# Optimization experiments

Hardware: AMD Instinct MI355X
Metric: run time of the kernel (lower is better)

## Reference

```python
import jax, jax.numpy as jnp
import numpy as np

# dims
B, F, K = 64, 4096, 8
D_IN = D_SLOT = D_KVQ = 192
HID = 768
N_ITERS = 3
EPS = 1e-8
GROUPS = [(0, 1), (1, 7), (7, 8)]  # bg / fg / ag contiguous slot slices
SB_STRENGTH = 1.0
SB_SIGMA = 0.25
GRID = 64  # sqrt(F)


def _layernorm(x, g, b):
    m = jnp.mean(x, axis=-1, keepdims=True)
    v = jnp.mean(jnp.square(x - m), axis=-1, keepdims=True)
    return (x - m) * jax.lax.rsqrt(v + 1e-5) * g + b


def _gru_cell(x, h, Wih, Whh, bih, bhh):
    # torch.nn.GRUCell semantics; gate order r, z, n
    gi = x @ Wih.T + bih
    gh = h @ Whh.T + bhh
    ir, iz, i_n = jnp.split(gi, 3, axis=-1)
    hr, hz, h_n = jnp.split(gh, 3, axis=-1)
    r = jax.nn.sigmoid(ir + hr)
    z = jax.nn.sigmoid(iz + hz)
    n = jnp.tanh(i_n + r * h_n)
    return (1.0 - z) * n + z * h


def _token_coords():
    y = np.linspace(-1.0, 1.0, GRID, dtype=np.float32)
    x = np.linspace(-1.0, 1.0, GRID, dtype=np.float32)
    yy, xx = np.meshgrid(y, x, indexing='ij')
    return jnp.asarray(np.stack((xx, yy), axis=-1).reshape(F, 2))


def setup_inputs() -> dict:
    key = jax.random.key(0)
    ks = jax.random.split(key, 16)
    def n(i, shape, s=0.02):
        return jax.random.normal(ks[i], shape, jnp.float32) * s
    return dict(
        features=jax.random.normal(ks[0], (B, F, D_IN), jnp.float32),
        slots=jax.random.normal(ks[1], (B, K, D_SLOT), jnp.float32),
        Wk=n(2, (D_IN, D_KVQ)), Wv=n(3, (D_IN, D_KVQ)), Wq=n(4, (D_SLOT, D_KVQ)),
        ln_feat_g=jnp.ones(D_IN), ln_feat_b=jnp.zeros(D_IN),
        ln_slot_g=jnp.ones(D_SLOT), ln_slot_b=jnp.zeros(D_SLOT),
        gru_Wih=n(5, (3, 3 * D_SLOT, D_KVQ)), gru_Whh=n(6, (3, 3 * D_SLOT, D_SLOT)),
        gru_bih=n(7, (3, 3 * D_SLOT)), gru_bhh=n(8, (3, 3 * D_SLOT)),
        mlp_ln_g=jnp.ones((3, D_SLOT)), mlp_ln_b=jnp.zeros((3, D_SLOT)),
        mlp_W1=n(9, (3, D_SLOT, HID)), mlp_b1=n(10, (3, HID)),
        mlp_W2=n(11, (3, HID, D_SLOT)), mlp_b2=n(12, (3, D_SLOT)),
    )


def reference(features, slots, Wk, Wv, Wq, ln_feat_g, ln_feat_b, ln_slot_g,
              ln_slot_b, gru_Wih, gru_Whh, gru_bih, gru_bhh, mlp_ln_g,
              mlp_ln_b, mlp_W1, mlp_b1, mlp_W2, mlp_b2):
    coords = _token_coords()  # (F, 2)
    f = _layernorm(features, ln_feat_g, ln_feat_b)
    k = f @ Wk  # (B, F, Dk)
    v = f @ Wv
    scale = D_KVQ ** -0.5
    sigma2 = max(SB_SIGMA ** 2, 1e-8)
    prev_attn = None
    for _ in range(N_ITERS):
        slots_prev = slots
        q = _layernorm(slots, ln_slot_g, ln_slot_b) @ Wq  # (B, K, Dk)
        dots = jnp.einsum('bkd,bfd->bkf', q, k) * scale
        if prev_attn is not None and SB_STRENGTH > 0.0:
            w = prev_attn / (prev_attn.sum(-1, keepdims=True) + 1e-8)
            centers = jnp.einsum('bkf,fd->bkd', w, coords)  # (B, K, 2)
            diff = coords[None, None] - centers[:, :, None]  # (B, K, F, 2)
            dist2 = jnp.sum(diff * diff, axis=-1)
            dots = dots + SB_STRENGTH * (-dist2 / (2.0 * sigma2))
        attn = jax.nn.softmax(dots, axis=1)  # competition over slots
        prev_attn = attn
        w = attn / (attn.sum(-1, keepdims=True) + EPS)  # weighted mean over F
        updates = jnp.einsum('bkf,bfd->bkd', w, v)  # (B, K, Dk)
        outs = []
        for g, (s, e) in enumerate(GROUPS):
            u = updates[:, s:e].reshape(-1, D_KVQ)
            h_prev = slots_prev[:, s:e].reshape(-1, D_SLOT)
            h = _gru_cell(u, h_prev, gru_Wih[g], gru_Whh[g], gru_bih[g], gru_bhh[g])
            x = _layernorm(h, mlp_ln_g[g], mlp_ln_b[g])
            x = jax.nn.relu(x @ mlp_W1[g] + mlp_b1[g]) @ mlp_W2[g] + mlp_b2[g]
            outs.append((h + x).reshape(B, e - s, D_SLOT))
        slots = jnp.concatenate(outs, axis=1)
    return slots
```

## Files before the change

### kernel.cpp

```cpp
#include <hip/hip_runtime.h>

typedef unsigned short u16;
typedef unsigned int u32;

#define BB 64
#define FF 4096
#define DD 192
#define HH 768

typedef __attribute__((ext_vector_type(8))) __bf16 bf16x8;
typedef __attribute__((ext_vector_type(4))) float f32x4;

__device__ __forceinline__ float bf2f(u32 u) {
  union { u32 i; float f; } x; x.i = u << 16; return x.f;
}
__device__ __forceinline__ u16 f2bf(float f) {
  __bf16 h = (__bf16)f;
  return __builtin_bit_cast(u16, h);
}
__device__ __forceinline__ u32 pk2bf(float a, float b) {
  return (u32)f2bf(a) | ((u32)f2bf(b) << 16);
}
__device__ __forceinline__ float sigm(float x) { return 1.f / (1.f + __expf(-x)); }

__global__ void prep_vw(const float* __restrict__ Wk, const float* __restrict__ Wv,
                        const float* __restrict__ g, const float* __restrict__ bb,
                        float* __restrict__ Wvm, float* __restrict__ s0v,
                        float* __restrict__ s0k) {
  int d = threadIdx.x;
  float av = 0.f, ak = 0.f;
  for (int e = 0; e < DD; ++e) {
    float wv = Wv[e * DD + d];
    Wvm[e * DD + d] = g[e] * wv;
    av += bb[e] * wv;
    ak += bb[e] * Wk[e * DD + d];
  }
  s0v[d] = av; s0k[d] = ak;
}

__global__ void prep_packw(const float* __restrict__ Wih, const float* __restrict__ Whh,
                           const float* __restrict__ W1, const float* __restrict__ W2,
                           u16* __restrict__ pWih, u16* __restrict__ pWhh,
                           u16* __restrict__ pW1, u16* __restrict__ pW2) {
  int which = blockIdx.y;
  int total, N, E;
  const float* src; u16* dst; int srcEmajor;
  if (which < 2) { total = 3 * 576 * 192; N = 576; E = 192; srcEmajor = 0;
                   src = which ? Whh : Wih; dst = which ? pWhh : pWih; }
  else if (which == 2) { total = 3 * 192 * 768; N = 768; E = 192; srcEmajor = 1;
                         src = W1; dst = pW1; }
  else { total = 3 * 768 * 192; N = 192; E = 768; srcEmajor = 1; src = W2; dst = pW2; }
  for (int idx = blockIdx.x * 256 + threadIdx.x; idx < total; idx += gridDim.x * 256) {
    int g = idx / (N * E), rem = idx % (N * E);
    int n, e;
    if (srcEmajor) { e = rem / N; n = rem % N; }
    else { n = rem / E; e = rem % E; }
    dst[((g * (E / 2) + (e >> 1)) * N + n) * 2 + (e & 1)] = f2bf(src[idx]);
  }
}

__global__ __launch_bounds__(256) void fconv(const float* __restrict__ feat,
                                             u16* __restrict__ fb, u16* __restrict__ fd,
                                             float2* __restrict__ stats) {
  __shared__ __align__(16) u16 flds[64 * 192];
  int tid = threadIdx.x;
  int blk = blockIdx.x;
  int r = tid >> 2, p = tid & 3;
  long t = (long)blk * 64 + r;
  const float4* src = (const float4*)(feat + t * DD) + p * 12;
  float s = 0.f, s2 = 0.f;
  long Tg = t >> 4; int tau = (int)(t & 15);
  #pragma unroll
  for (int i = 0; i < 6; ++i) {
    float4 a = src[i * 2], b = src[i * 2 + 1];
    s += a.x + a.y + a.z + a.w + b.x + b.y + b.z + b.w;
    s2 += a.x * a.x + a.y * a.y + a.z * a.z + a.w * a.w +
          b.x * b.x + b.y * b.y + b.z * b.z + b.w * b.w;
    uint4 v;
    v.x = pk2bf(a.x, a.y); v.y = pk2bf(a.z, a.w);
    v.z = pk2bf(b.x, b.y); v.w = pk2bf(b.z, b.w);
    int u = p * 6 + i;
    *(uint4*)(fb + ((Tg * 24 + u) * 16 + tau) * 8) = v;
    *(uint4*)((char*)flds + r * 384 + p * 96 + i * 16) = v;
  }
  s += __shfl_xor(s, 1); s2 += __shfl_xor(s2, 1);
  s += __shfl_xor(s, 2); s2 += __shfl_xor(s2, 2);
  if (p == 0) {
    float mu = s * (1.f / 192.f);
    float rstd = rsqrtf(s2 * (1.f / 192.f) - mu * mu + 1e-5f);
    stats[t] = make_float2(rstd, mu);
  }
  __syncthreads();
  int b = blk >> 6;
  #pragma unroll
  for (int i = 0; i < 6; ++i) {
    int idx = tid + i * 256;
    int tg8 = idx / 192, d = idx % 192;
    u16 h[8];
    #pragma unroll
    for (int j = 0; j < 8; ++j) h[j] = flds[(tg8 * 8 + j) * 192 + d];
    uint4 v;
    v.x = (u32)h[0] | ((u32)h[1] << 16);
    v.y = (u32)h[2] | ((u32)h[3] << 16);
    v.z = (u32)h[4] | ((u32)h[5] << 16);
    v.w = (u32)h[6] | ((u32)h[7] << 16);
    int g32 = (blk & 63) * 2 + (tg8 >> 2);
    int l4f = tg8 & 3;
    *(uint4*)(fd + ((((long)b * 128 + g32) * 12 + (d >> 4)) * 64 + l4f * 16 +
                    (d & 15)) * 8) = v;
  }
}

__global__ __launch_bounds__(64) void qproj_kernel(
    const float* __restrict__ slots, const float* __restrict__ Wq,
    const float* __restrict__ lsg, const float* __restrict__ lsb,
    const float* __restrict__ Wk, const float* __restrict__ lfg,
    const float* __restrict__ s0k,
    u16* __restrict__ pbuf, float* __restrict__ pab,
    float* __restrict__ U, float* __restrict__ scal_cur) {
  __shared__ float ln[192];
  int bk = blockIdx.x;
  int b = bk >> 3, sl = bk & 7;
  int lane = threadIdx.x;
  {
    int gtid = bk * 64 + lane;
    float4 z = {0.f, 0.f, 0.f, 0.f};
    if (gtid < 24576) ((float4*)U)[gtid] = z;
    else if (gtid < 24576 + 512) ((float4*)scal_cur)[gtid - 24576] = z;
  }
  const float* x = slots + bk * DD;
  float v0 = x[lane], v1 = x[lane + 64], v2 = x[lane + 128];
  float s = v0 + v1 + v2, s2 = v0 * v0 + v1 * v1 + v2 * v2;
  #pragma unroll
  for (int m = 1; m < 64; m <<= 1) { s += __shfl_xor(s, m); s2 += __shfl_xor(s2, m); }
  float mu = s * (1.f / 192.f);
  float rstd = rsqrtf(s2 * (1.f / 192.f) - mu * mu + 1e-5f);
  ln[lane]       = (v0 - mu) * rstd * lsg[lane]       + lsb[lane];
  ln[lane + 64]  = (v1 - mu) * rstd * lsg[lane + 64]  + lsb[lane + 64];
  ln[lane + 128] = (v2 - mu) * rstd * lsg[lane + 128] + lsb[lane + 128];
  __syncthreads();
  float a0 = 0.f, a1 = 0.f, a2 = 0.f;
  for (int e = 0; e < DD; ++e) {
    float le = ln[e];
    a0 += le * Wq[e * DD + lane];
    a1 += le * Wq[e * DD + lane + 64];
    a2 += le * Wq[e * DD + lane + 128];
  }
  __syncthreads();
  const float scale = 0.07216878364870323f;
  ln[lane] = a0 * scale; ln[lane + 64] = a1 * scale; ln[lane + 128] = a2 * scale;
  __syncthreads();
  float al = 0.f, be = 0.f;
  u16 pb[3];
  #pragma unroll
  for (int k3 = 0; k3 < 3; ++k3) {
    int d = lane + k3 * 64;
    const float* wr = Wk + (size_t)d * DD;
    float pd = 0.f;
    for (int e = 0; e < DD; ++e) pd += wr[e] * ln[e];
    pd *= lfg[d];
    u16 h = f2bf(pd);
    pb[k3] = h;
    al += bf2f(h);
    be += s0k[d] * ln[d];
  }
  #pragma unroll
  for (int m = 1; m < 64; m <<= 1) { al += __shfl_xor(al, m); be += __shfl_xor(be, m); }
  #pragma unroll
  for (int k3 = 0; k3 < 3; ++k3)
    pbuf[(b * 16 + sl) * DD + lane + k3 * 64] = pb[k3];
  if (lane < 24) *(uint4*)(pbuf + (b * 16 + 8 + sl) * DD + lane * 8) = (uint4){0, 0, 0, 0};
  if (lane == 0) { pab[bk * 2] = al; pab[bk * 2 + 1] = be; }
}

__global__ __launch_bounds__(256) void attnpv_kernel(
    const u16* __restrict__ fb, const u16* __restrict__ fd,
    const u16* __restrict__ pbuf, const float* __restrict__ pab,
    const float2* __restrict__ stats,
    const float* __restrict__ scal_prev,
    float* __restrict__ U, float* __restrict__ scal_cur, int have_bias) {
  __shared__ __align__(16) u16 plds[16 * 192];
  __shared__ __align__(16) u16 attn_lds[16 * 256];
  int b = blockIdx.x;
  int chunk = blockIdx.y * 256;
  int tid = threadIdx.x;
  #pragma unroll
  for (int i = 0; i < 2; ++i) {
    int g = tid + i * 256;
    if (g < 384) {
      int s = g / 24, u = g % 24;
      uint4 v = *(const uint4*)(pbuf + ((b * 16 + s) * DD + u * 8));
      *(uint4*)((char*)plds + s * 384 + ((u ^ (s & 7)) << 4)) = v;
    }
  }
  *(uint4*)((char*)attn_lds + 4096 + tid * 16) = (uint4){0, 0, 0, 0};
  __syncthreads();
  int w = tid >> 6, lane = tid & 63;
  int l15 = lane & 15, l4 = lane >> 4;
  bf16x8 qfr[6];
  #pragma unroll
  for (int kk = 0; kk < 6; ++kk) {
    int u = kk * 4 + l4;
    qfr[kk] = *(bf16x8*)((char*)plds + l15 * 384 + ((u ^ (l15 & 7)) << 4));
  }
  float ax[4], ay[4], c0[4], av[4], bv[4];
  #pragma unroll
  for (int j = 0; j < 4; ++j) {
    int s = l4 * 4 + j;
    if (s < 8) {
      av[j] = pab[(b * 8 + s) * 2];
      bv[j] = pab[(b * 8 + s) * 2 + 1];
      if (have_bias) {
        float inv = 1.f / (scal_prev[(b * 8 + s) * 4] + 1e-8f);
        float cx = scal_prev[(b * 8 + s) * 4 + 1] * inv;
        float cy = scal_prev[(b * 8 + s) * 4 + 2] * inv;
        ax[j] = 16.f * cx; ay[j] = 16.f * cy; c0[j] = -8.f * (cx * cx + cy * cy);
      } else { ax[j] = 0.f; ay[j] = 0.f; c0[j] = 0.f; }
    } else { av[j] = 0.f; bv[j] = 0.f; ax[j] = 0.f; ay[j] = 0.f; c0[j] = 0.f; }
  }
  float pa[4], px[4], py[4], pg[4];
  #pragma unroll
  for (int j = 0; j < 4; ++j) { pa[j] = 0.f; px[j] = 0.f; py[j] = 0.f; pg[j] = 0.f; }
  for (int tile = w; tile < 16; tile += 4) {
    int t0 = chunk + tile * 16;
    long Tg = (long)b * 256 + (t0 >> 4);
    const u16* kp = fb + (Tg * 24 + l4) * 128 + l15 * 8;
    f32x4 acc = (f32x4){0.f, 0.f, 0.f, 0.f};
    #pragma unroll
    for (int kk = 0; kk < 6; ++kk) {
      bf16x8 bfr = *(const bf16x8*)(kp + kk * 512);
      acc = __builtin_amdgcn_mfma_f32_16x16x32_bf16(qfr[kk], bfr, acc, 0, 0, 0);
    }
    int t = t0 + l15;
    float2 st = stats[((long)b << 12) + t];
    float rstd = st.x, muv = st.y;
    float x = -1.f + (float)(t & 63) * (2.f / 63.f);
    float y = -1.f + (float)(t >> 6) * (2.f / 63.f);
    float m8r2 = -8.f * (x * x + y * y);
    float d4[4];
    #pragma unroll
    for (int j = 0; j < 4; ++j)
      d4[j] = rstd * acc[j] - rstd * muv * av[j] + bv[j] +
              (have_bias ? (ax[j] * x + ay[j] * y + c0[j] + m8r2) : 0.f);
    float o4[4];
    #pragma unroll
    for (int j = 0; j < 4; ++j) o4[j] = __shfl_xor(d4[j], 16);
    float mx = fmaxf(fmaxf(fmaxf(d4[0], d4[1]), fmaxf(d4[2], d4[3])),
                     fmaxf(fmaxf(o4[0], o4[1]), fmaxf(o4[2], o4[3])));
    float e4[4];
    float sum = 0.f;
    #pragma unroll
    for (int j = 0; j < 4; ++j) { e4[j] = __expf(d4[j] - mx); sum += e4[j]; }
    #pragma unroll
    for (int j = 0; j < 4; ++j) sum += __expf(o4[j] - mx);
    float inv = 1.f / sum;
    if (l4 < 2) {
      int tl = tile * 16 + l15;
      #pragma unroll
      for (int j = 0; j < 4; ++j) {
        float a = e4[j] * inv;
        u16 wr = f2bf(a * rstd);
        int s = l4 * 4 + j;
        *(u16*)((char*)attn_lds + ((s * 512 + tl * 2) ^ ((s & 7) << 4))) = wr;
        pa[j] += a; px[j] += a * x; py[j] += a * y;
        pg[j] += bf2f(wr) * muv;
      }
    }
  }
  #pragma unroll
  for (int m = 1; m < 16; m <<= 1) {
    #pragma unroll
    for (int j = 0; j < 4; ++j) {
      pa[j] += __shfl_xor(pa[j], m);
      px[j] += __shfl_xor(px[j], m);
      py[j] += __shfl_xor(py[j], m);
      pg[j] += __shfl_xor(pg[j], m);
    }
  }
  if (l15 == 0 && l4 < 2) {
    #pragma unroll
    for (int j = 0; j < 4; ++j) {
      int s = l4 * 4 + j;
      atomicAdd(&scal_cur[(b * 8 + s) * 4], pa[j]);
      atomicAdd(&scal_cur[(b * 8 + s) * 4 + 1], px[j]);
      atomicAdd(&scal_cur[(b * 8 + s) * 4 + 2], py[j]);
      atomicAdd(&scal_cur[(b * 8 + s) * 4 + 3], pg[j]);
    }
  }
  __syncthreads();
  int g32base = chunk >> 5;
  #pragma unroll
  for (int ni = 0; ni < 3; ++ni) {
    int nt = w * 3 + ni;
    f32x4 acc = (f32x4){0.f, 0.f, 0.f, 0.f};
    const u16* vp = fd + ((((long)b * 128 + g32base) * 12 + nt) * 64 + l4 * 16 + l15) * 8;
    #pragma unroll
    for (int gl = 0; gl < 8; ++gl) {
      int tl0 = gl * 32 + l4 * 8;
      bf16x8 afr = *(bf16x8*)((char*)attn_lds + ((l15 * 512 + tl0 * 2) ^ ((l15 & 7) << 4)));
      bf16x8 bfr = *(const bf16x8*)(vp + gl * 12 * 64 * 8);
      acc = __builtin_amdgcn_mfma_f32_16x16x32_bf16(afr, bfr, acc, 0, 0, 0);
    }
    if (l4 < 2) {
      #pragma unroll
      for (int j = 0; j < 4; ++j) {
        int s = l4 * 4 + j;
        atomicAdd(&U[((long)b * 8 + s) * DD + nt * 16 + l15], acc[j]);
      }
    }
  }
}

template <int M>
__device__ void gru_body(int b0, int g, int srow,
                         float* u_l, float* h_l, float* gi_l, float* gh_l,
                         float* hn_l, float* ln_l, float* x1_l, float* out_l, float* st,
                         const float* __restrict__ U, const float* __restrict__ scal,
                         const float* __restrict__ Wvm, const float* __restrict__ s0v,
                         const float* __restrict__ sin_,
                         const u16* __restrict__ pWih, const u16* __restrict__ pWhh,
                         const float* __restrict__ bih, const float* __restrict__ bhh,
                         const float* __restrict__ mlng, const float* __restrict__ mlnb,
                         const u16* __restrict__ pW1, const float* __restrict__ b1,
                         const u16* __restrict__ pW2, const float* __restrict__ b2,
                         float* __restrict__ sout) {
  int tid = threadIdx.x;
  for (int idx = tid; idx < M * 192; idx += 768) {
    int row = idx / 192, d = idx % 192;
    int gr = b0 * 8 + srow + row;
    hn_l[row * 192 + d] = U[(long)gr * DD + d];
    h_l[row * 192 + d] = sin_[gr * DD + d];
  }
  __syncthreads();
  if (tid < M * 192) {
    int row = tid / 192, d = tid % 192;
    int gr = b0 * 8 + srow + row;
    float asum = scal[gr * 4], gam = scal[gr * 4 + 3];
    float inv = 1.f / (asum + 1e-8f);
    float acc = asum * s0v[d];
    const float* ur = hn_l + row * 192;
    #pragma unroll 4
    for (int e = 0; e < DD; ++e) acc += (ur[e] - gam) * Wvm[e * DD + d];
    u_l[row * 192 + d] = acc * inv;
  }
  __syncthreads();
  if (tid < 576) {
    int c = tid;
    const u16* wih = pWih + (size_t)g * 96 * 1152 + c * 2;
    const u16* whh = pWhh + (size_t)g * 96 * 1152 + c * 2;
    float ai[M], ah[M];
    #pragma unroll
    for (int r = 0; r < M; ++r) { ai[r] = 0.f; ah[r] = 0.f; }
    #pragma unroll 4
    for (int e2 = 0; e2 < 96; ++e2) {
      u32 wi = *(const u32*)(wih + e2 * 1152);
      u32 wh = *(const u32*)(whh + e2 * 1152);
      float wi0 = bf2f(wi & 0xffffu), wi1 = bf2f(wi >> 16);
      float wh0 = bf2f(wh & 0xffffu), wh1 = bf2f(wh >> 16);
      #pragma unroll
      for (int r = 0; r < M; ++r) {
        ai[r] += wi0 * u_l[r * 192 + e2 * 2] + wi1 * u_l[r * 192 + e2 * 2 + 1];
        ah[r] += wh0 * h_l[r * 192 + e2 * 2] + wh1 * h_l[r * 192 + e2 * 2 + 1];
      }
    }
    #pragma unroll
    for (int r = 0; r < M; ++r) { gi_l[r * 576 + c] = ai[r]; gh_l[r * 576 + c] = ah[r]; }
  }
  __syncthreads();
  if (tid < M * 192) {
    int row = tid / 192, uu = tid % 192;
    const float* bihg = bih + g * 576;
    const float* bhhg = bhh + g * 576;
    float r_ = sigm(gi_l[row * 576 + uu] + bihg[uu] + gh_l[row * 576 + uu] + bhhg[uu]);
    float z_ = sigm(gi_l[row * 576 + 192 + uu] + bihg[192 + uu] +
                    gh_l[row * 576 + 192 + uu] + bhhg[192 + uu]);
    float nn = gi_l[row * 576 + 384 + uu] + bihg[384 + uu] +
               r_ * (gh_l[row * 576 + 384 + uu] + bhhg[384 + uu]);
    float t = 1.f - 2.f / (__expf(2.f * nn) + 1.f);
    hn_l[row * 192 + uu] = (1.f - z_) * t + z_ * h_l[row * 192 + uu];
  }
  __syncthreads();
  {
    int wv = tid >> 6, lane = tid & 63;
    if (wv < M) {
      float v0 = hn_l[wv * 192 + lane], v1 = hn_l[wv * 192 + lane + 64],
            v2 = hn_l[wv * 192 + lane + 128];
      float s = v0 + v1 + v2, sq = v0 * v0 + v1 * v1 + v2 * v2;
      #pragma unroll
      for (int m = 1; m < 64; m <<= 1) { s += __shfl_xor(s, m); sq += __shfl_xor(sq, m); }
      if (lane == 0) {
        float mu = s * (1.f / 192.f);
        st[wv * 2] = mu;
        st[wv * 2 + 1] = rsqrtf(sq * (1.f / 192.f) - mu * mu + 1e-5f);
      }
    }
  }
  __syncthreads();
  if (tid < M * 192) {
    int row = tid / 192, uu = tid % 192;
    ln_l[row * 192 + uu] = (hn_l[row * 192 + uu] - st[row * 2]) * st[row * 2 + 1] *
                               mlng[g * DD + uu] + mlnb[g * DD + uu];
  }
  __syncthreads();
  {
    int c = tid;
    const u16* w1 = pW1 + (size_t)g * 96 * 1536 + c * 2;
    float a[M];
    #pragma unroll
    for (int r = 0; r < M; ++r) a[r] = 0.f;
    #pragma unroll 4
    for (int e2 = 0; e2 < 96; ++e2) {
      u32 wp = *(const u32*)(w1 + e2 * 1536);
      float w0 = bf2f(wp & 0xffffu), w1f = bf2f(wp >> 16);
      #pragma unroll
      for (int r = 0; r < M; ++r)
        a[r] += w0 * ln_l[r * 192 + e2 * 2] + w1f * ln_l[r * 192 + e2 * 2 + 1];
    }
    float bc = b1[g * HH + c];
    #pragma unroll
    for (int r = 0; r < M; ++r) x1_l[r * 768 + c] = fmaxf(a[r] + bc, 0.f);
  }
  if (tid < M * 192) {
    int row = tid / 192, uu = tid % 192;
    out_l[row * 192 + uu] = hn_l[row * 192 + uu] + b2[g * DD + uu];
  }
  __syncthreads();
  {
    int c = tid % 192, ks = tid / 192;
    const u16* w2 = pW2 + (size_t)g * 384 * 384 + c * 2;
    float a[M];
    #pragma unroll
    for (int r = 0; r < M; ++r) a[r] = 0.f;
    #pragma unroll 4
    for (int e2 = ks * 96; e2 < ks * 96 + 96; ++e2) {
      u32 wp = *(const u32*)(w2 + e2 * 384);
      float w0 = bf2f(wp & 0xffffu), w1f = bf2f(wp >> 16);
      #pragma unroll
      for (int r = 0; r < M; ++r)
        a[r] += w0 * x1_l[r * 768 + e2 * 2] + w1f * x1_l[r * 768 + e2 * 2 + 1];
    }
    #pragma unroll
    for (int r = 0; r < M; ++r) atomicAdd(&out_l[r * 192 + c], a[r]);
  }
  __syncthreads();
  if (tid < M * 192) {
    int row = tid / 192, d = tid % 192;
    sout[(b0 * 8 + srow + row) * DD + d] = out_l[row * 192 + d];
  }
}

__global__ __launch_bounds__(768) void gru_kernel(
    const float* __restrict__ U, const float* __restrict__ scal,
    const float* __restrict__ Wvm, const float* __restrict__ s0v,
    const float* __restrict__ sin_,
    const u16* __restrict__ pWih, const u16* __restrict__ pWhh,
    const float* __restrict__ bih, const float* __restrict__ bhh,
    const float* __restrict__ mlng, const float* __restrict__ mlnb,
    const u16* __restrict__ pW1, const float* __restrict__ b1,
    const u16* __restrict__ pW2, const float* __restrict__ b2,
    float* __restrict__ sout) {
  __shared__ float u_l[3 * 192], h_l[3 * 192], gi_l[3 * 576], gh_l[3 * 576];
  __shared__ float hn_l[3 * 192], ln_l[3 * 192], x1_l[3 * 768], out_l[3 * 192], st[8];
  int b = blockIdx.x, y = blockIdx.y;
  if (y == 0)
    gru_body<1>(b, 0, 0, u_l, h_l, gi_l, gh_l, hn_l, ln_l, x1_l, out_l, st,
                U, scal, Wvm, s0v, sin_, pWih, pWhh, bih, bhh, mlng, mlnb,
                pW1, b1, pW2, b2, sout);
  else if (y == 1)
    gru_body<1>(b, 2, 7, u_l, h_l, gi_l, gh_l, hn_l, ln_l, x1_l, out_l, st,
                U, scal, Wvm, s0v, sin_, pWih, pWhh, bih, bhh, mlng, mlnb,
                pW1, b1, pW2, b2, sout);
  else if (y == 2)
    gru_body<3>(b, 1, 1, u_l, h_l, gi_l, gh_l, hn_l, ln_l, x1_l, out_l, st,
                U, scal, Wvm, s0v, sin_, pWih, pWhh, bih, bhh, mlng, mlnb,
                pW1, b1, pW2, b2, sout);
  else
    gru_body<3>(b, 1, 4, u_l, h_l, gi_l, gh_l, hn_l, ln_l, x1_l, out_l, st,
                U, scal, Wvm, s0v, sin_, pWih, pWhh, bih, bhh, mlng, mlnb,
                pW1, b1, pW2, b2, sout);
}

extern "C" void kernel_launch(void* const* d_in, const int* in_sizes, int n_in,
                              void* d_out, int out_size, void* d_ws, size_t ws_size,
                              hipStream_t stream) {
  const float* feat = (const float*)d_in[0];
  const float* slots = (const float*)d_in[1];
  const float* Wk = (const float*)d_in[2];
  const float* Wv = (const float*)d_in[3];
  const float* Wq = (const float*)d_in[4];
  const float* lfg = (const float*)d_in[5];
  const float* lfb = (const float*)d_in[6];
  const float* lsg = (const float*)d_in[7];
  const float* lsb = (const float*)d_in[8];
  const float* gWih = (const float*)d_in[9];
  const float* gWhh = (const float*)d_in[10];
  const float* gbih = (const float*)d_in[11];
  const float* gbhh = (const float*)d_in[12];
  const float* mlng = (const float*)d_in[13];
  const float* mlnb = (const float*)d_in[14];
  const float* W1 = (const float*)d_in[15];
  const float* b1 = (const float*)d_in[16];
  const float* W2 = (const float*)d_in[17];
  const float* b2 = (const float*)d_in[18];
  float* out = (float*)d_out;

  char* ws = (char*)d_ws;
  size_t off = 0;
  auto alloc = [&](size_t bytes) {
    void* p = ws + off;
    off += (bytes + 255) & ~(size_t)255;
    return p;
  };
  u16* fb      = (u16*)alloc((size_t)BB * FF * DD * 2);
  u16* fd      = (u16*)alloc((size_t)BB * DD * FF * 2);
  float2* stats = (float2*)alloc((size_t)BB * FF * 8);
  u16* pbuf    = (u16*)alloc((size_t)BB * 16 * DD * 2);
  float* pab   = (float*)alloc((size_t)BB * 8 * 2 * 4);
  float* U     = (float*)alloc((size_t)BB * 8 * DD * 4);
  float* slA   = (float*)alloc((size_t)BB * 8 * DD * 4);
  float* slB   = (float*)alloc((size_t)BB * 8 * DD * 4);
  float* scal0 = (float*)alloc(BB * 8 * 4 * 4);
  float* scal1 = (float*)alloc(BB * 8 * 4 * 4);
  float* Wvm   = (float*)alloc((size_t)DD * DD * 4);
  float* s0v   = (float*)alloc(DD * 4);
  float* s0k   = (float*)alloc(DD * 4);
  u16* pWih    = (u16*)alloc((size_t)3 * 576 * DD * 2);
  u16* pWhh    = (u16*)alloc((size_t)3 * 576 * DD * 2);
  u16* pW1     = (u16*)alloc((size_t)3 * DD * HH * 2);
  u16* pW2     = (u16*)alloc((size_t)3 * HH * DD * 2);

  prep_vw<<<1, 192, 0, stream>>>(Wk, Wv, lfg, lfb, Wvm, s0v, s0k);
  prep_packw<<<dim3(432, 4), 256, 0, stream>>>(gWih, gWhh, W1, W2, pWih, pWhh, pW1, pW2);
  fconv<<<BB * FF / 64, 256, 0, stream>>>(feat, fb, fd, stats);

  const float* sin_ = slots;
  float* souts[3] = {slA, slB, out};
  float* scals[2] = {scal0, scal1};
  for (int it = 0; it < 3; ++it) {
    int cur = it & 1, prev = cur ^ 1;
    qproj_kernel<<<BB * 8, 64, 0, stream>>>(sin_, Wq, lsg, lsb, Wk, lfg, s0k,
                                            pbuf, pab, U, scals[cur]);
    attnpv_kernel<<<dim3(BB, 16), 256, 0, stream>>>(fb, fd, pbuf, pab, stats,
                                                    scals[prev], U, scals[cur],
                                                    it > 0 ? 1 : 0);
    gru_kernel<<<dim3(BB, 4), 768, 0, stream>>>(U, scals[cur], Wvm, s0v, sin_,
                                                pWih, pWhh, gbih, gbhh, mlng, mlnb,
                                                pW1, b1, pW2, b2, souts[it]);
    sin_ = souts[it];
  }
}
```

Measured before the change: 519.2 us.

## Fuse first-iteration attention and PV into feature conversion kernel

Merges the first slot-attention iteration (logits, softmax over slots, attention-weighted value accumulation, centroid scalars) into the feature bf16 conversion kernel, so the freshly converted 64-token tile in LDS is reused instead of re-read from global memory. The first qproj launch is moved before the conversion kernel, and the remaining iterations always apply the spatial bias, so the have_bias flag is dropped. In exchange, the fused kernel uses more LDS and registers and adds more atomics per block into U and the scalar buffers.

Result: slower. 774.7 us (+49.2%).

```diff
diff --git a/kernel.cpp b/kernel.cpp
--- a/kernel.cpp
+++ b/kernel.cpp
@@ -59,55 +59,180 @@
   }
 }
 
-__global__ __launch_bounds__(256) void fconv(const float* __restrict__ feat,
-                                             u16* __restrict__ fb, u16* __restrict__ fd,
-                                             float2* __restrict__ stats) {
+__global__ __launch_bounds__(256) void fconv_attn1(
+    const float* __restrict__ feat, u16* __restrict__ fb, u16* __restrict__ fd,
+    float2* __restrict__ stats, const u16* __restrict__ pbuf,
+    const float* __restrict__ pab, float* __restrict__ U,
+    float* __restrict__ scal_cur) {
   __shared__ __align__(16) u16 flds[64 * 192];
+  __shared__ __align__(16) u16 plds[16 * 192];
+  __shared__ __align__(16) u16 attn_lds[16 * 64];
+  __shared__ float stat_l[64 * 2];
   int tid = threadIdx.x;
   int blk = blockIdx.x;
-  int r = tid >> 2, p = tid & 3;
-  long t = (long)blk * 64 + r;
-  const float4* src = (const float4*)(feat + t * DD) + p * 12;
-  float s = 0.f, s2 = 0.f;
-  long Tg = t >> 4; int tau = (int)(t & 15);
+  int b = blk >> 6;
+  int w = tid >> 6, lane = tid & 63;
+  int l15 = lane & 15, l4 = lane >> 4;
+  #pragma unroll
+  for (int i = 0; i < 2; ++i) {
+    int g = tid + i * 256;
+    if (g < 384) {
+      int s = g / 24, u = g % 24;
+      uint4 v = *(const uint4*)(pbuf + ((b * 16 + s) * DD + u * 8));
+      *(uint4*)((char*)plds + s * 384 + ((u ^ (s & 7)) << 4)) = v;
+    }
+  }
+  if (tid < 64) *(uint4*)((char*)attn_lds + 1024 + tid * 16) = (uint4){0, 0, 0, 0};
+  {
+    int r = tid >> 2, p = tid & 3;
+    long t = (long)blk * 64 + r;
+    const float4* src = (const float4*)(feat + t * DD) + p * 12;
+    float s = 0.f, s2 = 0.f;
+    long Tg = t >> 4; int tau = (int)(t & 15);
+    #pragma unroll
+    for (int i = 0; i < 6; ++i) {
+      float4 a = src[i * 2], c = src[i * 2 + 1];
+      s += a.x + a.y + a.z + a.w + c.x + c.y + c.z + c.w;
+      s2 += a.x * a.x + a.y * a.y + a.z * a.z + a.w * a.w +
+            c.x * c.x + c.y * c.y + c.z * c.z + c.w * c.w;
+      uint4 v;
+      v.x = pk2bf(a.x, a.y); v.y = pk2bf(a.z, a.w);
+      v.z = pk2bf(c.x, c.y); v.w = pk2bf(c.z, c.w);
+      int u = p * 6 + i;
+      *(uint4*)(fb + ((Tg * 24 + u) * 16 + tau) * 8) = v;
+      *(uint4*)((char*)flds + r * 384 + ((u ^ (r & 7)) << 4)) = v;
+    }
+    s += __shfl_xor(s, 1); s2 += __shfl_xor(s2, 1);
+    s += __shfl_xor(s, 2); s2 += __shfl_xor(s2, 2);
+    if (p == 0) {
+      float mu = s * (1.f / 192.f);
+      float rstd = rsqrtf(s2 * (1.f / 192.f) - mu * mu + 1e-5f);
+      stats[t] = make_float2(rstd, mu);
+      stat_l[r * 2] = rstd; stat_l[r * 2 + 1] = mu;
+    }
+  }
+  __syncthreads();
+  uint4 gran[6];
   #pragma unroll
   for (int i = 0; i < 6; ++i) {
-    float4 a = src[i * 2], b = src[i * 2 + 1];
-    s += a.x + a.y + a.z + a.w + b.x + b.y + b.z + b.w;
-    s2 += a.x * a.x + a.y * a.y + a.z * a.z + a.w * a.w +
-          b.x * b.x + b.y * b.y + b.z * b.z + b.w * b.w;
-    uint4 v;
-    v.x = pk2bf(a.x, a.y); v.y = pk2bf(a.z, a.w);
-    v.z = pk2bf(b.x, b.y); v.w = pk2bf(b.z, b.w);
-    int u = p * 6 + i;
-    *(uint4*)(fb + ((Tg * 24 + u) * 16 + tau) * 8) = v;
-    *(uint4*)((char*)flds + r * 384 + p * 96 + i * 16) = v;
-  }
-  s += __shfl_xor(s, 1); s2 += __shfl_xor(s2, 1);
-  s += __shfl_xor(s, 2); s2 += __shfl_xor(s2, 2);
-  if (p == 0) {
-    float mu = s * (1.f / 192.f);
-    float rstd = rsqrtf(s2 * (1.f / 192.f) - mu * mu + 1e-5f);
-    stats[t] = make_float2(rstd, mu);
-  }
-  __syncthreads();
-  int b = blk >> 6;
-  #pragma unroll
-  for (int i = 0; i < 6; ++i) {
-    int idx = tid + i * 256;
-    int tg8 = idx / 192, d = idx % 192;
+    int pair = w * 6 + i;
+    int nt = pair >> 1, ks = pair & 1;
+    int d = nt * 16 + l15;
     u16 h[8];
     #pragma unroll
-    for (int j = 0; j < 8; ++j) h[j] = flds[(tg8 * 8 + j) * 192 + d];
+    for (int j = 0; j < 8; ++j) {
+      int tok = ks * 32 + l4 * 8 + j;
+      h[j] = *(const u16*)((char*)flds + tok * 384 +
+                           (((d >> 3) ^ (tok & 7)) << 4) + (d & 7) * 2);
+    }
     uint4 v;
     v.x = (u32)h[0] | ((u32)h[1] << 16);
     v.y = (u32)h[2] | ((u32)h[3] << 16);
     v.z = (u32)h[4] | ((u32)h[5] << 16);
     v.w = (u32)h[6] | ((u32)h[7] << 16);
-    int g32 = (blk & 63) * 2 + (tg8 >> 2);
-    int l4f = tg8 & 3;
-    *(uint4*)(fd + ((((long)b * 128 + g32) * 12 + (d >> 4)) * 64 + l4f * 16 +
-                    (d & 15)) * 8) = v;
+    gran[i] = v;
+    int g32 = (blk & 63) * 2 + ks;
+    *(uint4*)(fd + ((((long)b * 128 + g32) * 12 + nt) * 64 + l4 * 16 + l15) * 8) = v;
+  }
+  bf16x8 qfr[6];
+  #pragma unroll
+  for (int kk = 0; kk < 6; ++kk) {
+    int u = kk * 4 + l4;
+    qfr[kk] = *(bf16x8*)((char*)plds + l15 * 384 + ((u ^ (l15 & 7)) << 4));
+  }
+  float av[4], bv[4];
+  #pragma unroll
+  for (int j = 0; j < 4; ++j) {
+    int s = l4 * 4 + j;
+    av[j] = (s < 8) ? pab[(b * 8 + s) * 2] : 0.f;
+    bv[j] = (s < 8) ? pab[(b * 8 + s) * 2 + 1] : 0.f;
+  }
+  {
+    int tl = w * 16 + l15;
+    f32x4 acc = (f32x4){0.f, 0.f, 0.f, 0.f};
+    #pragma unroll
+    for (int kk = 0; kk < 6; ++kk) {
+      int u = kk * 4 + l4;
+      bf16x8 bfr = *(bf16x8*)((char*)flds + tl * 384 + ((u ^ (tl & 7)) << 4));
+      acc = __builtin_amdgcn_mfma_f32_16x16x32_bf16(qfr[kk], bfr, acc, 0, 0, 0);
+    }
+    float rstd = stat_l[tl * 2], muv = stat_l[tl * 2 + 1];
+    int t = (blk & 63) * 64 + tl;
+    float x = -1.f + (float)(t & 63) * (2.f / 63.f);
+    float y = -1.f + (float)(t >> 6) * (2.f / 63.f);
+    float d4[4];
+    #pragma unroll
+    for (int j = 0; j < 4; ++j)
+      d4[j] = rstd * acc[j] - rstd * muv * av[j] + bv[j];
+    float o4[4];
+    #pragma unroll
+    for (int j = 0; j < 4; ++j) o4[j] = __shfl_xor(d4[j], 16);
+    float mx = fmaxf(fmaxf(fmaxf(d4[0], d4[1]), fmaxf(d4[2], d4[3])),
+                     fmaxf(fmaxf(o4[0], o4[1]), fmaxf(o4[2], o4[3])));
+    float e4[4];
+    float sum = 0.f;
+    #pragma unroll
+    for (int j = 0; j < 4; ++j) { e4[j] = __expf(d4[j] - mx); sum += e4[j]; }
+    #pragma unroll
+    for (int j = 0; j < 4; ++j) sum += __expf(o4[j] - mx);
+    float inv = 1.f / sum;
+    float pa[4], px[4], py[4], pg[4];
+    #pragma unroll
+    for (int j = 0; j < 4; ++j) { pa[j] = 0.f; px[j] = 0.f; py[j] = 0.f; pg[j] = 0.f; }
+    if (l4 < 2) {
+      #pragma unroll
+      for (int j = 0; j < 4; ++j) {
+        float a = e4[j] * inv;
+        u16 wr = f2bf(a * rstd);
+        int s = l4 * 4 + j;
+        *(u16*)((char*)attn_lds + ((s * 128 + tl * 2) ^ ((s & 7) << 4))) = wr;
+        pa[j] = a; px[j] = a * x; py[j] = a * y;
+        pg[j] = bf2f(wr) * muv;
+      }
+    }
+    #pragma unroll
+    for (int m = 1; m < 16; m <<= 1) {
+      #pragma unroll
+      for (int j = 0; j < 4; ++j) {
+        pa[j] += __shfl_xor(pa[j], m);
+        px[j] += __shfl_xor(px[j], m);
+        py[j] += __shfl_xor(py[j], m);
+        pg[j] += __shfl_xor(pg[j], m);
+      }
+    }
+    if (l15 == 0 && l4 < 2) {
+      #pragma unroll
+      for (int j = 0; j < 4; ++j) {
+        int s = l4 * 4 + j;
+        atomicAdd(&scal_cur[(b * 8 + s) * 4], pa[j]);
+        atomicAdd(&scal_cur[(b * 8 + s) * 4 + 1], px[j]);
+        atomicAdd(&scal_cur[(b * 8 + s) * 4 + 2], py[j]);
+        atomicAdd(&scal_cur[(b * 8 + s) * 4 + 3], pg[j]);
+      }
+    }
+  }
+  __syncthreads();
+  f32x4 pacc[3];
+  #pragma unroll
+  for (int ni = 0; ni < 3; ++ni) pacc[ni] = (f32x4){0.f, 0.f, 0.f, 0.f};
+  #pragma unroll
+  for (int i = 0; i < 6; ++i) {
+    int ks = (w * 6 + i) & 1;
+    int tl0 = ks * 32 + l4 * 8;
+    bf16x8 afr = *(bf16x8*)((char*)attn_lds + ((l15 * 128 + tl0 * 2) ^ ((l15 & 7) << 4)));
+    pacc[i >> 1] = __builtin_amdgcn_mfma_f32_16x16x32_bf16(
+        afr, __builtin_bit_cast(bf16x8, gran[i]), pacc[i >> 1], 0, 0, 0);
+  }
+  if (l4 < 2) {
+    #pragma unroll
+    for (int ni = 0; ni < 3; ++ni) {
+      int nt = w * 3 + ni;
+      #pragma unroll
+      for (int j = 0; j < 4; ++j) {
+        int s = l4 * 4 + j;
+        atomicAdd(&U[((long)b * 8 + s) * DD + nt * 16 + l15], pacc[ni][j]);
+      }
+    }
   }
 }
 
@@ -178,7 +303,7 @@
     const u16* __restrict__ pbuf, const float* __restrict__ pab,
     const float2* __restrict__ stats,
     const float* __restrict__ scal_prev,
-    float* __restrict__ U, float* __restrict__ scal_cur, int have_bias) {
+    float* __restrict__ U, float* __restrict__ scal_cur) {
   __shared__ __align__(16) u16 plds[16 * 192];
   __shared__ __align__(16) u16 attn_lds[16 * 256];
   int b = blockIdx.x;
@@ -210,12 +335,10 @@
     if (s < 8) {
       av[j] = pab[(b * 8 + s) * 2];
       bv[j] = pab[(b * 8 + s) * 2 + 1];
-      if (have_bias) {
-        float inv = 1.f / (scal_prev[(b * 8 + s) * 4] + 1e-8f);
-        float cx = scal_prev[(b * 8 + s) * 4 + 1] * inv;
-        float cy = scal_prev[(b * 8 + s) * 4 + 2] * inv;
-        ax[j] = 16.f * cx; ay[j] = 16.f * cy; c0[j] = -8.f * (cx * cx + cy * cy);
-      } else { ax[j] = 0.f; ay[j] = 0.f; c0[j] = 0.f; }
+      float inv = 1.f / (scal_prev[(b * 8 + s) * 4] + 1e-8f);
+      float cx = scal_prev[(b * 8 + s) * 4 + 1] * inv;
+      float cy = scal_prev[(b * 8 + s) * 4 + 2] * inv;
+      ax[j] = 16.f * cx; ay[j] = 16.f * cy; c0[j] = -8.f * (cx * cx + cy * cy);
     } else { av[j] = 0.f; bv[j] = 0.f; ax[j] = 0.f; ay[j] = 0.f; c0[j] = 0.f; }
   }
   float pa[4], px[4], py[4], pg[4];
@@ -241,7 +364,7 @@
     #pragma unroll
     for (int j = 0; j < 4; ++j)
       d4[j] = rstd * acc[j] - rstd * muv * av[j] + bv[j] +
-              (have_bias ? (ax[j] * x + ay[j] * y + c0[j] + m8r2) : 0.f);
+              ax[j] * x + ay[j] * y + c0[j] + m8r2;
     float o4[4];
     #pragma unroll
     for (int j = 0; j < 4; ++j) o4[j] = __shfl_xor(d4[j], 16);
@@ -531,18 +654,24 @@
 
   prep_vw<<<1, 192, 0, stream>>>(Wk, Wv, lfg, lfb, Wvm, s0v, s0k);
   prep_packw<<<dim3(432, 4), 256, 0, stream>>>(gWih, gWhh, W1, W2, pWih, pWhh, pW1, pW2);
-  fconv<<<BB * FF / 64, 256, 0, stream>>>(feat, fb, fd, stats);
-
-  const float* sin_ = slots;
+
   float* souts[3] = {slA, slB, out};
   float* scals[2] = {scal0, scal1};
-  for (int it = 0; it < 3; ++it) {
+
+  qproj_kernel<<<BB * 8, 64, 0, stream>>>(slots, Wq, lsg, lsb, Wk, lfg, s0k,
+                                          pbuf, pab, U, scals[0]);
+  fconv_attn1<<<BB * FF / 64, 256, 0, stream>>>(feat, fb, fd, stats, pbuf, pab,
+                                                U, scals[0]);
+  gru_kernel<<<dim3(BB, 4), 768, 0, stream>>>(U, scals[0], Wvm, s0v, slots,
+                                              pWih, pWhh, gbih, gbhh, mlng, mlnb,
+                                              pW1, b1, pW2, b2, souts[0]);
+  const float* sin_ = souts[0];
+  for (int it = 1; it < 3; ++it) {
     int cur = it & 1, prev = cur ^ 1;
     qproj_kernel<<<BB * 8, 64, 0, stream>>>(sin_, Wq, lsg, lsb, Wk, lfg, s0k,
                                             pbuf, pab, U, scals[cur]);
     attnpv_kernel<<<dim3(BB, 16), 256, 0, stream>>>(fb, fd, pbuf, pab, stats,
-                                                    scals[prev], U, scals[cur],
-                                                    it > 0 ? 1 : 0);
+                                                    scals[prev], U, scals[cur]);
     gru_kernel<<<dim3(BB, 4), 768, 0, stream>>>(U, scals[cur], Wvm, s0v, sin_,
                                                 pWih, pWhh, gbih, gbhh, mlng, mlnb,
                                                 pW1, b1, pW2, b2, souts[it]);
```

## Fuse next-iteration query projection into GRU kernel and replace U atomics with partials

Applied to the files above, without the earlier changes.

The per-iteration qproj kernel is removed, except for the first iteration. Each GRU block now computes LayerNorm, the Wq projection and the Wk-folded query for its own output slots, and it zeroes the next scal buffer. The attention-PV kernel writes per-chunk partial sums into a U_part buffer instead of doing atomicAdd into U, and the GRU kernel sums the 16 chunks when it loads. This removes two kernel launches, the U zeroing and the atomic contention. In exchange the GRU tail does a serial matvec per block and reads a 16x larger partial buffer.

Result: no change. 513.4 us (-1.1%).

```diff
diff --git a/kernel.cpp b/kernel.cpp
--- a/kernel.cpp
+++ b/kernel.cpp
@@ -117,16 +117,14 @@
     const float* __restrict__ Wk, const float* __restrict__ lfg,
     const float* __restrict__ s0k,
     u16* __restrict__ pbuf, float* __restrict__ pab,
-    float* __restrict__ U, float* __restrict__ scal_cur) {
+    float* __restrict__ scal_cur) {
   __shared__ float ln[192];
   int bk = blockIdx.x;
   int b = bk >> 3, sl = bk & 7;
   int lane = threadIdx.x;
   {
     int gtid = bk * 64 + lane;
-    float4 z = {0.f, 0.f, 0.f, 0.f};
-    if (gtid < 24576) ((float4*)U)[gtid] = z;
-    else if (gtid < 24576 + 512) ((float4*)scal_cur)[gtid - 24576] = z;
+    if (gtid < 512) ((float4*)scal_cur)[gtid] = (float4){0.f, 0.f, 0.f, 0.f};
   }
   const float* x = slots + bk * DD;
   float v0 = x[lane], v1 = x[lane + 64], v2 = x[lane + 128];
@@ -178,11 +176,11 @@
     const u16* __restrict__ pbuf, const float* __restrict__ pab,
     const float2* __restrict__ stats,
     const float* __restrict__ scal_prev,
-    float* __restrict__ U, float* __restrict__ scal_cur, int have_bias) {
+    float* __restrict__ U_part, float* __restrict__ scal_cur, int have_bias) {
   __shared__ __align__(16) u16 plds[16 * 192];
   __shared__ __align__(16) u16 attn_lds[16 * 256];
-  int b = blockIdx.x;
-  int chunk = blockIdx.y * 256;
+  int b = blockIdx.x, cy = blockIdx.y;
+  int chunk = cy * 256;
   int tid = threadIdx.x;
   #pragma unroll
   for (int i = 0; i < 2; ++i) {
@@ -213,8 +211,8 @@
       if (have_bias) {
         float inv = 1.f / (scal_prev[(b * 8 + s) * 4] + 1e-8f);
         float cx = scal_prev[(b * 8 + s) * 4 + 1] * inv;
-        float cy = scal_prev[(b * 8 + s) * 4 + 2] * inv;
-        ax[j] = 16.f * cx; ay[j] = 16.f * cy; c0[j] = -8.f * (cx * cx + cy * cy);
+        float cy2 = scal_prev[(b * 8 + s) * 4 + 2] * inv;
+        ax[j] = 16.f * cx; ay[j] = 16.f * cy2; c0[j] = -8.f * (cx * cx + cy2 * cy2);
       } else { ax[j] = 0.f; ay[j] = 0.f; c0[j] = 0.f; }
     } else { av[j] = 0.f; bv[j] = 0.f; ax[j] = 0.f; ay[j] = 0.f; c0[j] = 0.f; }
   }
@@ -289,6 +287,7 @@
   }
   __syncthreads();
   int g32base = chunk >> 5;
+  float* up = U_part + (size_t)(b * 16 + cy) * 1536;
   #pragma unroll
   for (int ni = 0; ni < 3; ++ni) {
     int nt = w * 3 + ni;
@@ -303,10 +302,8 @@
     }
     if (l4 < 2) {
       #pragma unroll
-      for (int j = 0; j < 4; ++j) {
-        int s = l4 * 4 + j;
-        atomicAdd(&U[((long)b * 8 + s) * DD + nt * 16 + l15], acc[j]);
-      }
+      for (int j = 0; j < 4; ++j)
+        up[(l4 * 4 + j) * 192 + nt * 16 + l15] = acc[j];
     }
   }
 }
@@ -315,7 +312,7 @@
 __device__ void gru_body(int b0, int g, int srow,
                          float* u_l, float* h_l, float* gi_l, float* gh_l,
                          float* hn_l, float* ln_l, float* x1_l, float* out_l, float* st,
-                         const float* __restrict__ U, const float* __restrict__ scal,
+                         const float* __restrict__ U_part, const float* __restrict__ scal,
                          const float* __restrict__ Wvm, const float* __restrict__ s0v,
                          const float* __restrict__ sin_,
                          const u16* __restrict__ pWih, const u16* __restrict__ pWhh,
@@ -323,12 +320,21 @@
                          const float* __restrict__ mlng, const float* __restrict__ mlnb,
                          const u16* __restrict__ pW1, const float* __restrict__ b1,
                          const u16* __restrict__ pW2, const float* __restrict__ b2,
-                         float* __restrict__ sout) {
+                         float* __restrict__ sout,
+                         const float* __restrict__ Wq, const float* __restrict__ lsg,
+                         const float* __restrict__ lsb, const float* __restrict__ Wk,
+                         const float* __restrict__ lfg, const float* __restrict__ s0k,
+                         u16* __restrict__ pbuf, float* __restrict__ pab,
+                         float* __restrict__ scal_next, int do_tail) {
   int tid = threadIdx.x;
   for (int idx = tid; idx < M * 192; idx += 768) {
     int row = idx / 192, d = idx % 192;
     int gr = b0 * 8 + srow + row;
-    hn_l[row * 192 + d] = U[(long)gr * DD + d];
+    float acc = 0.f;
+    const float* upb = U_part + (size_t)b0 * 16 * 1536 + (srow + row) * 192 + d;
+    #pragma unroll 4
+    for (int c = 0; c < 16; ++c) acc += upb[c * 1536];
+    hn_l[row * 192 + d] = acc;
     h_l[row * 192 + d] = sin_[gr * DD + d];
   }
   __syncthreads();
@@ -447,10 +453,68 @@
     int row = tid / 192, d = tid % 192;
     sout[(b0 * 8 + srow + row) * DD + d] = out_l[row * 192 + d];
   }
+  if (!do_tail) return;
+  if (tid < M * 4) scal_next[(b0 * 8 + srow + tid / 4) * 4 + (tid & 3)] = 0.f;
+  if (tid >= 64 && tid < 64 + 2 * M) st[8 + (tid - 64)] = 0.f;
+  {
+    int wv = tid >> 6, lane = tid & 63;
+    if (wv < M) {
+      float v0 = out_l[wv * 192 + lane], v1 = out_l[wv * 192 + lane + 64],
+            v2 = out_l[wv * 192 + lane + 128];
+      float s = v0 + v1 + v2, sq = v0 * v0 + v1 * v1 + v2 * v2;
+      #pragma unroll
+      for (int m = 1; m < 64; m <<= 1) { s += __shfl_xor(s, m); sq += __shfl_xor(sq, m); }
+      if (lane == 0) {
+        float mu = s * (1.f / 192.f);
+        st[wv * 2] = mu;
+        st[wv * 2 + 1] = rsqrtf(sq * (1.f / 192.f) - mu * mu + 1e-5f);
+      }
+    }
+  }
+  __syncthreads();
+  if (tid < M * 192) {
+    int row = tid / 192, d = tid % 192;
+    ln_l[row * 192 + d] = (out_l[row * 192 + d] - st[row * 2]) * st[row * 2 + 1] *
+                              lsg[d] + lsb[d];
+  }
+  __syncthreads();
+  if (tid < M * 192) {
+    int row = tid / 192, d = tid % 192;
+    float q = 0.f;
+    #pragma unroll 4
+    for (int e = 0; e < DD; ++e) q += ln_l[row * 192 + e] * Wq[e * DD + d];
+    gi_l[row * 192 + d] = q * 0.07216878364870323f;
+  }
+  __syncthreads();
+  if (tid < M * 192) {
+    int row = tid / 192, d = tid % 192;
+    const float* wr = Wk + (size_t)d * DD;
+    const float* qr = gi_l + row * 192;
+    float pd = 0.f;
+    #pragma unroll 4
+    for (int e = 0; e < DD; ++e) pd += wr[e] * qr[e];
+    pd *= lfg[d];
+    u16 h = f2bf(pd);
+    pbuf[(b0 * 16 + srow + row) * DD + d] = h;
+    float al = bf2f(h);
+    float be = s0k[d] * qr[d];
+    #pragma unroll
+    for (int m = 1; m < 64; m <<= 1) { al += __shfl_xor(al, m); be += __shfl_xor(be, m); }
+    if ((tid & 63) == 0) {
+      atomicAdd(&st[8 + row * 2], al);
+      atomicAdd(&st[9 + row * 2], be);
+    }
+  }
+  __syncthreads();
+  if (tid < M) {
+    int bk = b0 * 8 + srow + tid;
+    pab[bk * 2] = st[8 + tid * 2];
+    pab[bk * 2 + 1] = st[9 + tid * 2];
+  }
 }
 
 __global__ __launch_bounds__(768) void gru_kernel(
-    const float* __restrict__ U, const float* __restrict__ scal,
+    const float* __restrict__ U_part, const float* __restrict__ scal,
     const float* __restrict__ Wvm, const float* __restrict__ s0v,
     const float* __restrict__ sin_,
     const u16* __restrict__ pWih, const u16* __restrict__ pWhh,
@@ -458,26 +522,35 @@
     const float* __restrict__ mlng, const float* __restrict__ mlnb,
     const u16* __restrict__ pW1, const float* __restrict__ b1,
     const u16* __restrict__ pW2, const float* __restrict__ b2,
-    float* __restrict__ sout) {
+    float* __restrict__ sout,
+    const float* __restrict__ Wq, const float* __restrict__ lsg,
+    const float* __restrict__ lsb, const float* __restrict__ Wk,
+    const float* __restrict__ lfg, const float* __restrict__ s0k,
+    u16* __restrict__ pbuf, float* __restrict__ pab,
+    float* __restrict__ scal_next, int do_tail) {
   __shared__ float u_l[3 * 192], h_l[3 * 192], gi_l[3 * 576], gh_l[3 * 576];
-  __shared__ float hn_l[3 * 192], ln_l[3 * 192], x1_l[3 * 768], out_l[3 * 192], st[8];
+  __shared__ float hn_l[3 * 192], ln_l[3 * 192], x1_l[3 * 768], out_l[3 * 192], st[16];
   int b = blockIdx.x, y = blockIdx.y;
   if (y == 0)
     gru_body<1>(b, 0, 0, u_l, h_l, gi_l, gh_l, hn_l, ln_l, x1_l, out_l, st,
-                U, scal, Wvm, s0v, sin_, pWih, pWhh, bih, bhh, mlng, mlnb,
-                pW1, b1, pW2, b2, sout);
+                U_part, scal, Wvm, s0v, sin_, pWih, pWhh, bih, bhh, mlng, mlnb,
+                pW1, b1, pW2, b2, sout, Wq, lsg, lsb, Wk, lfg, s0k,
+                pbuf, pab, scal_next, do_tail);
   else if (y == 1)
     gru_body<1>(b, 2, 7, u_l, h_l, gi_l, gh_l, hn_l, ln_l, x1_l, out_l, st,
-                U, scal, Wvm, s0v, sin_, pWih, pWhh, bih, bhh, mlng, mlnb,
-                pW1, b1, pW2, b2, sout);
+                U_part, scal, Wvm, s0v, sin_, pWih, pWhh, bih, bhh, mlng, mlnb,
+                pW1, b1, pW2, b2, sout, Wq, lsg, lsb, Wk, lfg, s0k,
+                pbuf, pab, scal_next, do_tail);
   else if (y == 2)
     gru_body<3>(b, 1, 1, u_l, h_l, gi_l, gh_l, hn_l, ln_l, x1_l, out_l, st,
-                U, scal, Wvm, s0v, sin_, pWih, pWhh, bih, bhh, mlng, mlnb,
-                pW1, b1, pW2, b2, sout);
+                U_part, scal, Wvm, s0v, sin_, pWih, pWhh, bih, bhh, mlng, mlnb,
+                pW1, b1, pW2, b2, sout, Wq, lsg, lsb, Wk, lfg, s0k,
+                pbuf, pab, scal_next, do_tail);
   else
     gru_body<3>(b, 1, 4, u_l, h_l, gi_l, gh_l, hn_l, ln_l, x1_l, out_l, st,
-                U, scal, Wvm, s0v, sin_, pWih, pWhh, bih, bhh, mlng, mlnb,
-                pW1, b1, pW2, b2, sout);
+                U_part, scal, Wvm, s0v, sin_, pWih, pWhh, bih, bhh, mlng, mlnb,
+                pW1, b1, pW2, b2, sout, Wq, lsg, lsb, Wk, lfg, s0k,
+                pbuf, pab, scal_next, do_tail);
 }
 
 extern "C" void kernel_launch(void* const* d_in, const int* in_sizes, int n_in,
@@ -511,41 +584,45 @@
     off += (bytes + 255) & ~(size_t)255;
     return p;
   };
-  u16* fb      = (u16*)alloc((size_t)BB * FF * DD * 2);
-  u16* fd      = (u16*)alloc((size_t)BB * DD * FF * 2);
+  u16* fb       = (u16*)alloc((size_t)BB * FF * DD * 2);
+  u16* fd       = (u16*)alloc((size_t)BB * DD * FF * 2);
   float2* stats = (float2*)alloc((size_t)BB * FF * 8);
-  u16* pbuf    = (u16*)alloc((size_t)BB * 16 * DD * 2);
-  float* pab   = (float*)alloc((size_t)BB * 8 * 2 * 4);
-  float* U     = (float*)alloc((size_t)BB * 8 * DD * 4);
-  float* slA   = (float*)alloc((size_t)BB * 8 * DD * 4);
-  float* slB   = (float*)alloc((size_t)BB * 8 * DD * 4);
-  float* scal0 = (float*)alloc(BB * 8 * 4 * 4);
-  float* scal1 = (float*)alloc(BB * 8 * 4 * 4);
-  float* Wvm   = (float*)alloc((size_t)DD * DD * 4);
-  float* s0v   = (float*)alloc(DD * 4);
-  float* s0k   = (float*)alloc(DD * 4);
-  u16* pWih    = (u16*)alloc((size_t)3 * 576 * DD * 2);
-  u16* pWhh    = (u16*)alloc((size_t)3 * 576 * DD * 2);
-  u16* pW1     = (u16*)alloc((size_t)3 * DD * HH * 2);
-  u16* pW2     = (u16*)alloc((size_t)3 * HH * DD * 2);
+  u16* pbuf     = (u16*)alloc((size_t)BB * 16 * DD * 2);
+  float* pab    = (float*)alloc((size_t)BB * 8 * 2 * 4);
+  float* U_part = (float*)alloc((size_t)BB * 16 * 8 * DD * 4);
+  float* slA    = (float*)alloc((size_t)BB * 8 * DD * 4);
+  float* slB    = (float*)alloc((size_t)BB * 8 * DD * 4);
+  float* scal0  = (float*)alloc(BB * 8 * 4 * 4);
+  float* scal1  = (float*)alloc(BB * 8 * 4 * 4);
+  float* Wvm    = (float*)alloc((size_t)DD * DD * 4);
+  float* s0v    = (float*)alloc(DD * 4);
+  float* s0k    = (float*)alloc(DD * 4);
+  u16* pWih     = (u16*)alloc((size_t)3 * 576 * DD * 2);
+  u16* pWhh     = (u16*)alloc((size_t)3 * 576 * DD * 2);
+  u16* pW1      = (u16*)alloc((size_t)3 * DD * HH * 2);
+  u16* pW2      = (u16*)alloc((size_t)3 * HH * DD * 2);
 
   prep_vw<<<1, 192, 0, stream>>>(Wk, Wv, lfg, lfb, Wvm, s0v, s0k);
   prep_packw<<<dim3(432, 4), 256, 0, stream>>>(gWih, gWhh, W1, W2, pWih, pWhh, pW1, pW2);
   fconv<<<BB * FF / 64, 256, 0, stream>>>(feat, fb, fd, stats);
 
-  const float* sin_ = slots;
   float* souts[3] = {slA, slB, out};
   float* scals[2] = {scal0, scal1};
+
+  qproj_kernel<<<BB * 8, 64, 0, stream>>>(slots, Wq, lsg, lsb, Wk, lfg, s0k,
+                                          pbuf, pab, scals[0]);
+  const float* sin_ = slots;
   for (int it = 0; it < 3; ++it) {
     int cur = it & 1, prev = cur ^ 1;
-    qproj_kernel<<<BB * 8, 64, 0, stream>>>(sin_, Wq, lsg, lsb, Wk, lfg, s0k,
-                                            pbuf, pab, U, scals[cur]);
     attnpv_kernel<<<dim3(BB, 16), 256, 0, stream>>>(fb, fd, pbuf, pab, stats,
-                                                    scals[prev], U, scals[cur],
+                                                    scals[prev], U_part, scals[cur],
                                                     it > 0 ? 1 : 0);
-    gru_kernel<<<dim3(BB, 4), 768, 0, stream>>>(U, scals[cur], Wvm, s0v, sin_,
+    gru_kernel<<<dim3(BB, 4), 768, 0, stream>>>(U_part, scals[cur], Wvm, s0v, sin_,
                                                 pWih, pWhh, gbih, gbhh, mlng, mlnb,
-                                                pW1, b1, pW2, b2, souts[it]);
+                                                pW1, b1, pW2, b2, souts[it],
+                                                Wq, lsg, lsb, Wk, lfg, s0k,
+                                                pbuf, pab, scals[prev],
+                                                it < 2 ? 1 : 0);
     sin_ = souts[it];
   }
 }
```
